# Performance work log

Hardware: AMD Instinct MI355X
Metric: run time of the kernel (lower is better)

The kernel has to match this reference:

```python
import jax, jax.numpy as jnp
import numpy as np

DIM = 256
HEADS = 8
HEAD_DIM = DIM // HEADS
B = 8
HH, WW = 32, 32
N = HH * WW
TABLE = (2 * HH - 1) * (2 * WW - 1)  # 3969
CPB_HID = 512


def _l2norm(t, eps=1e-12):
    # matches torch F.normalize(dim=-1): x / max(||x||, eps)
    n = jnp.sqrt(jnp.sum(t * t, axis=-1, keepdims=True))
    return t / jnp.maximum(n, eps)


def setup_inputs() -> dict:
    key = jax.random.key(0)
    ks = jax.random.split(key, 12)
    x = jax.random.normal(ks[0], (B, N, DIM), dtype=jnp.float32)
    relative_pos_index = jax.random.randint(ks[1], (N, N), 0, TABLE)
    relative_coords_table = jax.random.normal(ks[2], (TABLE, 2), dtype=jnp.float32)
    s = 0.02
    qkv_w = jax.random.normal(ks[3], (3 * DIM, DIM), dtype=jnp.float32) * s
    qkv_b = jnp.zeros((3 * DIM,), dtype=jnp.float32)
    query_embedding = jax.random.normal(ks[4], (HEADS, 1, HEAD_DIM), dtype=jnp.float32) * s
    # temperature init: log(exp(1/0.24) - 1) so softplus(temperature) = 1/0.24
    temperature = jnp.full((HEADS, 1, 1), float(np.log(np.expm1(1.0 / 0.24))), dtype=jnp.float32)
    proj_w = jax.random.normal(ks[5], (DIM, DIM), dtype=jnp.float32) * s
    proj_b = jnp.zeros((DIM,), dtype=jnp.float32)
    cpb_fc1_w = jax.random.normal(ks[6], (CPB_HID, 2), dtype=jnp.float32) * s
    cpb_fc1_b = jnp.zeros((CPB_HID,), dtype=jnp.float32)
    cpb_fc2_w = jax.random.normal(ks[7], (HEADS, CPB_HID), dtype=jnp.float32) * s
    cpb_fc2_b = jnp.zeros((HEADS,), dtype=jnp.float32)
    return dict(x=x, H=HH, W=WW, relative_pos_index=relative_pos_index,
                relative_coords_table=relative_coords_table,
                qkv_w=qkv_w, qkv_b=qkv_b, query_embedding=query_embedding,
                temperature=temperature, proj_w=proj_w, proj_b=proj_b,
                cpb_fc1_w=cpb_fc1_w, cpb_fc1_b=cpb_fc1_b,
                cpb_fc2_w=cpb_fc2_w, cpb_fc2_b=cpb_fc2_b)


def reference(x, H, W, relative_pos_index, relative_coords_table,
              qkv_w, qkv_b, query_embedding, temperature,
              proj_w, proj_b, cpb_fc1_w, cpb_fc1_b, cpb_fc2_w, cpb_fc2_b):
    Bc, Nc, C = x.shape
    seq_length_scale = jnp.asarray(np.log(HH * WW), dtype=x.dtype)  # from init input_resolution
    # qkv projection -> [B, heads, N, head_dim] each
    qkv = (x @ qkv_w.T + qkv_b).reshape(Bc, Nc, 3 * HEADS, HEAD_DIM).transpose(0, 2, 1, 3)
    q, k, v = qkv[:, :HEADS], qkv[:, HEADS:2 * HEADS], qkv[:, 2 * HEADS:]
    # CPB relative position bias: small MLP over coord table, then NxN gather
    h = jax.nn.relu(relative_coords_table @ cpb_fc1_w.T + cpb_fc1_b)  # [T, 512]
    table = (h @ cpb_fc2_w.T + cpb_fc2_b).T                           # [heads, T]
    rel_bias = table[:, relative_pos_index.reshape(-1)].reshape(HEADS, Nc, Nc)
    # cosine attention with learned temperature
    qn = _l2norm(q) + query_embedding[None]                           # [B, heads, N, hd]
    scale = jax.nn.softplus(temperature) * seq_length_scale           # [heads, 1, 1]
    attn = jnp.einsum('bhnd,bhmd->bhnm', qn * scale[None], _l2norm(k)) + rel_bias[None]
    attn = jax.nn.softmax(attn, axis=-1)
    out = jnp.einsum('bhnm,bhmd->bhnd', attn, v).transpose(0, 2, 1, 3).reshape(Bc, Nc, C)
    return out @ proj_w.T + proj_b
```

## Files before the change

kernel.cpp:

```cpp
#include <hip/hip_runtime.h>
#include <hip/hip_bf16.h>
#include <cstddef>
#include <cstdint>

typedef float v4f __attribute__((ext_vector_type(4)));
typedef short v8s __attribute__((ext_vector_type(8)));

__device__ __forceinline__ short f2bf(float x) {
    __hip_bfloat16 h = __float2bfloat16(x);
    short s; __builtin_memcpy(&s, &h, 2); return s;
}
__device__ __forceinline__ float bf2f(short s) {
    __hip_bfloat16 h; __builtin_memcpy(&h, &s, 2);
    return __bfloat162float(h);
}
__device__ __forceinline__ void gld16(const void* g, void* l) {
    __builtin_amdgcn_global_load_lds(
        (const __attribute__((address_space(1))) unsigned int*)g,
        (__attribute__((address_space(3))) unsigned int*)l, 16, 0, 0);
}
#define MFMA(a,b,c) __builtin_amdgcn_mfma_f32_16x16x32_bf16((a),(b),(c),0,0,0)

__global__ __launch_bounds__(256)
void cpb_kernel(const float* __restrict__ rct,
                const float* __restrict__ fc1w, const float* __restrict__ fc1b,
                const float* __restrict__ fc2w, const float* __restrict__ fc2b,
                float* __restrict__ table)
{
    __shared__ float s1[128];
    __shared__ float sb[64];
    __shared__ float s2[8][64];
    int tid = threadIdx.x;
    int jc  = blockIdx.y;
    int j0  = jc * 64;
    if (tid < 128) s1[tid] = fc1w[j0*2 + tid];
    else if (tid < 192) sb[tid-128] = fc1b[j0 + tid - 128];
    for (int i = tid; i < 512; i += 256) s2[i >> 6][i & 63] = fc2w[(i>>6)*512 + j0 + (i & 63)];
    __syncthreads();
    int r = blockIdx.x * 256 + tid;
    bool ok = r < 3969;
    float c0 = ok ? rct[2*r]   : 0.f;
    float c1 = ok ? rct[2*r+1] : 0.f;
    float a[8] = {0,0,0,0,0,0,0,0};
    #pragma unroll 4
    for (int j = 0; j < 64; ++j) {
        float hv = fmaxf(c0*s1[2*j] + c1*s1[2*j+1] + sb[j], 0.0f);
        #pragma unroll
        for (int hh = 0; hh < 8; ++hh) a[hh] += hv * s2[hh][j];
    }
    if (ok) {
        #pragma unroll
        for (int hh = 0; hh < 8; ++hh)
            atomicAdd(&table[hh*3969 + r], a[hh] + (jc == 0 ? fc2b[hh] : 0.f));
    }
}

__global__ __launch_bounds__(256)
void bias_mat(const float* __restrict__ tblf, const int* __restrict__ rpi,
              float* __restrict__ biasM)
{
    __shared__ float tb[3969];
    int h   = blockIdx.x >> 6;
    int q16 = blockIdx.x & 63;
    int tid = threadIdx.x;
    int w = tid >> 6, lane = tid & 63, t = lane & 15, quad = lane >> 4;
    for (int i = tid; i < 3969; i += 256) tb[i] = tblf[h*3969 + i];
    __syncthreads();
    int row0 = q16*16 + quad*4;
    #pragma unroll 1
    for (int kk = 0; kk < 4; ++kk) {
        int kt = w*4 + kk;
        #pragma unroll
        for (int g = 0; g < 4; ++g) {
            v4f o;
            #pragma unroll
            for (int r = 0; r < 4; ++r) {
                int idx = rpi[(size_t)(row0 + r)*1024 + kt*64 + 4*t + g];
                o[r] = tb[idx] - 40.0f;
            }
            size_t base = ((((size_t)(h*64 + q16)*16 + kt)*4 + g)*64 + lane)*4;
            *(v4f*)(biasM + base) = o;
        }
    }
}

__global__ __launch_bounds__(256)
void split_kernel(const float* __restrict__ x,  short* __restrict__ xh,  short* __restrict__ xl,
                  const float* __restrict__ wq, short* __restrict__ wqh, short* __restrict__ wql,
                  const float* __restrict__ wp, short* __restrict__ wph, short* __restrict__ wpl)
{
    int bid = blockIdx.x;
    const float* src; short* dh; short* dl; int base8;
    if (bid < 1024)      { src = x;  dh = xh;  dl = xl;  base8 = bid * 256; }
    else if (bid < 1120) { src = wq; dh = wqh; dl = wql; base8 = (bid-1024) * 256; }
    else                 { src = wp; dh = wph; dl = wpl; base8 = (bid-1120) * 256; }
    int e0 = (base8 + (int)threadIdx.x) * 8;
    int m  = e0 >> 8;
    int k  = e0 & 255;
    int kt = k >> 6, c = (k >> 3) & 7;
    float4 f0 = *(const float4*)(src + e0);
    float4 f1 = *(const float4*)(src + e0 + 4);
    float v[8] = {f0.x,f0.y,f0.z,f0.w,f1.x,f1.y,f1.z,f1.w};
    v8s hi, lo;
    #pragma unroll
    for (int j = 0; j < 8; ++j) {
        short h = f2bf(v[j]);
        hi[j] = h;
        lo[j] = f2bf(v[j] - bf2f(h));
    }
    int dst = m*256 + kt*64 + ((c ^ (m & 7)) << 3);
    *(v8s*)&dh[dst] = hi;
    *(v8s*)&dl[dst] = lo;
}

template<int MODE, int PASSES>
__global__ __launch_bounds__(256)
void gemm_mfma(const short* __restrict__ Ahi, const short* __restrict__ Alo,
               const short* __restrict__ Whi, const short* __restrict__ Wlo,
               const float* __restrict__ bias, float* __restrict__ C,
               short* __restrict__ qhi, short* __restrict__ qlo,
               short* __restrict__ khi, short* __restrict__ klo,
               short* __restrict__ vt,
               const float* __restrict__ qe, const float* __restrict__ temp,
               int N)
{
    __shared__ __align__(16) char smem[49152];
    short* Ah = (short*)smem;
    short* Al = Ah + 128*64;
    short* Wh = Al + 128*64;
    short* Wl = Wh + 64*64;

    int tid  = threadIdx.x;
    int w    = tid >> 6;
    int lane = tid & 63;
    int t    = lane & 15;
    int quad = lane >> 4;
    int m0 = blockIdx.y * 128, n0 = blockIdx.x * 64;
    int Mw = (w >> 1) * 64, Nw = (w & 1) * 32;
    const bool onep = (PASSES == 1) || (MODE == 1 && n0 >= 512);

    v4f acc[4][2];
    #pragma unroll
    for (int mt = 0; mt < 4; ++mt)
        #pragma unroll
        for (int nt = 0; nt < 2; ++nt) acc[mt][nt] = (v4f){0,0,0,0};

    int lr8 = lane >> 3, lc8 = lane & 7;
    #pragma unroll 1
    for (int kt = 0; kt < 4; ++kt) {
        __syncthreads();
        #pragma unroll
        for (int i = 0; i < 4; ++i) {
            size_t grow = (size_t)(m0 + w*32 + i*8 + lr8) * 256 + kt*64 + lc8*8;
            int ls = (w*32 + i*8) * 64;
            gld16(Ahi + grow, Ah + ls);
            if (!onep) gld16(Alo + grow, Al + ls);
        }
        #pragma unroll
        for (int i = 0; i < 2; ++i) {
            size_t grow = (size_t)(n0 + w*16 + i*8 + lr8) * 256 + kt*64 + lc8*8;
            int ls = (w*16 + i*8) * 64;
            gld16(Whi + grow, Wh + ls);
            if (!onep) gld16(Wlo + grow, Wl + ls);
        }
        __syncthreads();
        #pragma unroll
        for (int kk = 0; kk < 2; ++kk) {
            int cp = ((kk*4 + quad) ^ (t & 7)) << 3;
            v8s bh8[2], bl8[2];
            #pragma unroll
            for (int nt = 0; nt < 2; ++nt) {
                int rowi = Nw + nt*16 + t;
                bh8[nt] = *(const v8s*)&Wh[rowi*64 + cp];
                if (!onep) bl8[nt] = *(const v8s*)&Wl[rowi*64 + cp];
            }
            #pragma unroll
            for (int mt = 0; mt < 4; ++mt) {
                int rowi = Mw + mt*16 + t;
                v8s ah = *(const v8s*)&Ah[rowi*64 + cp];
                v8s al;
                if (!onep) al = *(const v8s*)&Al[rowi*64 + cp];
                #pragma unroll
                for (int nt = 0; nt < 2; ++nt) {
                    acc[mt][nt] = MFMA(ah, bh8[nt], acc[mt][nt]);
                    if (!onep) {
                        acc[mt][nt] = MFMA(al, bh8[nt], acc[mt][nt]);
                        acc[mt][nt] = MFMA(ah, bl8[nt], acc[mt][nt]);
                    }
                }
            }
        }
    }

    #pragma unroll
    for (int nt = 0; nt < 2; ++nt) {
        float bv = bias[n0 + Nw + nt*16 + t];
        #pragma unroll
        for (int mt = 0; mt < 4; ++mt)
            #pragma unroll
            for (int r = 0; r < 4; ++r) acc[mt][nt][r] += bv;
    }

    if (MODE == 0) {
        #pragma unroll
        for (int mt = 0; mt < 4; ++mt)
            #pragma unroll
            for (int r = 0; r < 4; ++r) {
                int m = m0 + Mw + mt*16 + quad*4 + r;
                #pragma unroll
                for (int nt = 0; nt < 2; ++nt) {
                    int n = n0 + Nw + nt*16 + t;
                    C[(size_t)m * N + n] = acc[mt][nt][r];
                }
            }
    } else {
        int which = n0 >> 8;
        if (which < 2) {
            int head = ((n0 + Nw) >> 5) & 7;
            float scale = 0.f;
            if (which == 0)
                scale = log1pf(__expf(temp[head])) * 6.9314718055994531f;
            #pragma unroll
            for (int mt = 0; mt < 4; ++mt)
                #pragma unroll
                for (int r = 0; r < 4; ++r) {
                    float a0 = acc[mt][0][r], a1 = acc[mt][1][r];
                    float s = a0*a0 + a1*a1;
                    s += __shfl_xor(s, 1); s += __shfl_xor(s, 2);
                    s += __shfl_xor(s, 4); s += __shfl_xor(s, 8);
                    float inv = 1.0f / fmaxf(sqrtf(s), 1e-12f);
                    int m = m0 + Mw + mt*16 + quad*4 + r;
                    int b = m >> 10, nrow = m & 1023;
                    if (which == 0) {
                        size_t rowoff = (((size_t)b*8 + head)*1024 + nrow) * 32;
                        #pragma unroll
                        for (int nt = 0; nt < 2; ++nt) {
                            int d = nt*16 + t;
                            float val = (acc[mt][nt][r] * inv + qe[head*32 + d]) * scale;
                            short hb = f2bf(val);
                            qhi[rowoff + d] = hb;
                            qlo[rowoff + d] = f2bf(val - bf2f(hb));
                        }
                    } else {
                        int kk = nrow & 63;
                        int p  = (kk & 3)*16 + (kk >> 2);
                        int prow = (nrow & ~63) | p;
                        int swk = (kk >> 3) & 3;
                        size_t rowoff = (((size_t)b*8 + head)*1024 + prow) * 32;
                        #pragma unroll
                        for (int nt = 0; nt < 2; ++nt) {
                            int d = nt*16 + t;
                            int c = d >> 3;
                            int dpos = ((c ^ swk) << 3) | (d & 7);
                            float val = acc[mt][nt][r] * inv;
                            short hb = f2bf(val);
                            khi[rowoff + dpos] = hb;
                            klo[rowoff + dpos] = f2bf(val - bf2f(hb));
                        }
                    }
                }
        } else {
            __syncthreads();
            short* VT = (short*)smem;
            #pragma unroll
            for (int mt = 0; mt < 4; ++mt)
                #pragma unroll
                for (int nt = 0; nt < 2; ++nt) {
                    int cl = Nw + nt*16 + t;
                    #pragma unroll
                    for (int r = 0; r < 4; ++r) {
                        int rl = Mw + mt*16 + quad*4 + r;
                        VT[cl*136 + rl] = f2bf(acc[mt][nt][r]);
                    }
                }
            __syncthreads();
            int b = m0 >> 10;
            int keybase = m0 & 1023;
            int headbase = ((n0 - 512) >> 5) & 7;
            int cl = tid >> 2;
            int dim = cl & 31;
            int hd  = headbase + (cl >> 5);
            size_t obase = (((size_t)b*8 + hd)*32 + dim) * 1024 + keybase;
            #pragma unroll
            for (int p = 0; p < 4; ++p) {
                int ci  = (tid & 3) * 4 + p;
                int ktl = ci >> 3, c = ci & 7;
                v8s val = *(const v8s*)&VT[cl*136 + ktl*64 + c*8];
                *(v8s*)&vt[obase + ktl*64 + ((c ^ (dim & 7)) << 3)] = val;
            }
        }
    }
}

__global__ __launch_bounds__(256)
void attn_mfma(const short* __restrict__ qhi, const short* __restrict__ qlo,
               const short* __restrict__ khi, const short* __restrict__ klo,
               const short* __restrict__ vt,  const float* __restrict__ biasM,
               short* __restrict__ yhi)
{
    __shared__ __align__(16) short Khi_s[2][2048];
    __shared__ __align__(16) short Klo_s[2][2048];
    __shared__ __align__(16) short Vt_s[2][2048];
    __shared__ __align__(16) short Ps[4][16][68];

    int bh  = blockIdx.x >> 4;
    int qt  = blockIdx.x & 15;
    int h   = bh & 7;
    int b   = bh >> 3;
    int tid = threadIdx.x;
    int w    = tid >> 6;
    int lane = tid & 63;
    int t    = lane & 15;
    int quad = lane >> 4;

    size_t qoff = ((size_t)bh*1024 + qt*64 + w*16 + t) * 32 + quad*8;
    v8s qfh = *(const v8s*)(qhi + qoff);
    v8s qfl = *(const v8s*)(qlo + qoff);

    v4f Oacc[2] = {{0,0,0,0},{0,0,0,0}};
    float lsum[4] = {0,0,0,0};

    size_t kgbase = (size_t)bh * 32768;
    const float* bmb = biasM + ((size_t)(h*64 + qt*4 + w) * 16) * 1024 + lane*4;
    int qrow0 = qt*64 + w*16 + quad*4;
    int swzS = (quad ^ ((t >> 1) & 3)) << 3;
    int lr8 = lane >> 3, lc8 = lane & 7;

    gld16(khi + kgbase + w*512 + lane*8, &Khi_s[0][w*512]);
    gld16(klo + kgbase + w*512 + lane*8, &Klo_s[0][w*512]);
    gld16(vt + kgbase + (size_t)(w*8 + lr8)*1024 + lc8*8, &Vt_s[0][w*512]);
    v4f curb[4];
    #pragma unroll
    for (int g = 0; g < 4; ++g) curb[g] = *(const v4f*)(bmb + g*256);

    #pragma unroll 1
    for (int kt = 0; kt < 16; ++kt) {
        int cur = kt & 1;
        __syncthreads();
        v4f nxtb[4];
        if (kt < 15) {
            int nkt = kt + 1, nb = cur ^ 1;
            gld16(khi + kgbase + (size_t)nkt*2048 + w*512 + lane*8, &Khi_s[nb][w*512]);
            gld16(klo + kgbase + (size_t)nkt*2048 + w*512 + lane*8, &Klo_s[nb][w*512]);
            gld16(vt + kgbase + (size_t)(w*8 + lr8)*1024 + nkt*64 + lc8*8, &Vt_s[nb][w*512]);
            const float* bp = bmb + (size_t)nkt*1024;
            #pragma unroll
            for (int g = 0; g < 4; ++g) nxtb[g] = *(const v4f*)(bp + g*256);
        }

        v4f S[4];
        #pragma unroll
        for (int g = 0; g < 4; ++g) {
            v8s bh8 = *(const v8s*)&Khi_s[cur][(g*16 + t)*32 + swzS];
            v8s bl8 = *(const v8s*)&Klo_s[cur][(g*16 + t)*32 + swzS];
            v4f c = curb[g];
            c = MFMA(qfh, bh8, c);
            c = MFMA(qfl, bh8, c);
            c = MFMA(qfh, bl8, c);
            S[g] = c;
        }

        #pragma unroll
        for (int r = 0; r < 4; ++r) {
            float p0 = __expf(S[0][r]);
            float p1 = __expf(S[1][r]);
            float p2 = __expf(S[2][r]);
            float p3 = __expf(S[3][r]);
            lsum[r] += (p0 + p1) + (p2 + p3);
            uint2 pk;
            pk.x = (uint32_t)(uint16_t)f2bf(p0) | ((uint32_t)(uint16_t)f2bf(p1) << 16);
            pk.y = (uint32_t)(uint16_t)f2bf(p2) | ((uint32_t)(uint16_t)f2bf(p3) << 16);
            *(uint2*)&Ps[w][quad*4 + r][t*4] = pk;
        }

        #pragma unroll
        for (int ks = 0; ks < 2; ++ks) {
            v8s pf = *(const v8s*)&Ps[w][t][ks*32 + quad*8];
            int vsw = ((ks*4 + quad) ^ (t & 7)) << 3;
            #pragma unroll
            for (int g = 0; g < 2; ++g) {
                v8s vf = *(const v8s*)&Vt_s[cur][(g*16 + t)*64 + vsw];
                Oacc[g] = MFMA(pf, vf, Oacc[g]);
            }
        }
        #pragma unroll
        for (int g = 0; g < 4; ++g) curb[g] = nxtb[g];
    }

    #pragma unroll
    for (int r = 0; r < 4; ++r) {
        float l = lsum[r];
        l += __shfl_xor(l, 1); l += __shfl_xor(l, 2);
        l += __shfl_xor(l, 4); l += __shfl_xor(l, 8);
        float inv = 1.0f / l;
        int qrow = qrow0 + r;
        int m = b*1024 + qrow;
        size_t mbase = (size_t)m * 256;
        int mk = m & 7;
        #pragma unroll
        for (int g = 0; g < 2; ++g) {
            float o = Oacc[g][r] * inv;
            int c = h*4 + g*2 + (t >> 3);
            int chp = ((c ^ mk) << 3) | (t & 7);
            yhi[mbase + chp] = f2bf(o);
        }
    }
}

extern "C" void kernel_launch(void* const* d_in, const int* in_sizes, int n_in,
                              void* d_out, int out_size, void* d_ws, size_t ws_size,
                              hipStream_t stream)
{
    const float* x     = (const float*)d_in[0];
    const int*   rpi   = (const int*)d_in[3];
    const float* rct   = (const float*)d_in[4];
    const float* qkvw  = (const float*)d_in[5];
    const float* qkvb  = (const float*)d_in[6];
    const float* qe    = (const float*)d_in[7];
    const float* temp  = (const float*)d_in[8];
    const float* projw = (const float*)d_in[9];
    const float* projb = (const float*)d_in[10];
    const float* fc1w  = (const float*)d_in[11];
    const float* fc1b  = (const float*)d_in[12];
    const float* fc2w  = (const float*)d_in[13];
    const float* fc2b  = (const float*)d_in[14];

    char* p = (char*)d_ws;
    float* tblf  = (float*)p;  p += 131072;
    short* xh    = (short*)p;  p += 4194304;
    short* xl    = (short*)p;  p += 4194304;
    short* wqh   = (short*)p;  p += 393216;
    short* wql   = (short*)p;  p += 393216;
    short* wph   = (short*)p;  p += 131072;
    short* wpl   = (short*)p;  p += 131072;
    short* qh    = (short*)p;  p += 4194304;
    short* ql    = (short*)p;  p += 4194304;
    short* kh    = (short*)p;  p += 4194304;
    short* kl    = (short*)p;  p += 4194304;
    short* vt    = (short*)p;  p += 4194304;
    float* biasM = (float*)p;  p += 33554432;
    float* out   = (float*)d_out;

    hipMemsetAsync(tblf, 0, 8*3969*sizeof(float), stream);
    cpb_kernel<<<dim3(16,8), 256, 0, stream>>>(rct, fc1w, fc1b, fc2w, fc2b, tblf);

    bias_mat<<<512, 256, 0, stream>>>(tblf, rpi, biasM);

    split_kernel<<<1152, 256, 0, stream>>>(x, xh, xl, qkvw, wqh, wql, projw, wph, wpl);

    dim3 g1(768/64, 8192/128);
    gemm_mfma<1,3><<<g1, 256, 0, stream>>>(xh, xl, wqh, wql, qkvb, nullptr,
                                           qh, ql, kh, kl, vt, qe, temp, 768);

    attn_mfma<<<1024, 256, 0, stream>>>(qh, ql, kh, kl, vt, biasM, xh);

    dim3 g2(256/64, 8192/128);
    gemm_mfma<0,1><<<g2, 256, 0, stream>>>(xh, nullptr, wph, nullptr, projb, out,
                                           nullptr, nullptr, nullptr, nullptr,
                                           nullptr, nullptr, nullptr, 256);
}
```

Baseline: 170.3 us.

## Store relative-position bias as bf16 and fold log2e into exp2 softmax

The precomputed per-head NxN bias matrix is now written and read as bf16 instead of fp32, with the constant -40 offset dropped. This halves its write and read traffic in the bias and attention kernels. Log2(e) is folded into the bias table and the query scale (6.93 becomes 10), so the attention kernel can use the native exp2 instruction in place of exp. Float-to-bf16 conversions use a cheaper add-and-shift rounding (round-half-up) with perm packing. The risks are lost bias precision, slightly different rounding, and larger exponent values now that the offset is gone.

```diff
diff --git a/kernel.cpp b/kernel.cpp
--- a/kernel.cpp
+++ b/kernel.cpp
@@ -6,20 +6,31 @@
 typedef float v4f __attribute__((ext_vector_type(4)));
 typedef short v8s __attribute__((ext_vector_type(8)));
 
-__device__ __forceinline__ short f2bf(float x) {
-    __hip_bfloat16 h = __float2bfloat16(x);
-    short s; __builtin_memcpy(&s, &h, 2); return s;
-}
-__device__ __forceinline__ float bf2f(short s) {
-    __hip_bfloat16 h; __builtin_memcpy(&h, &s, 2);
-    return __bfloat162float(h);
-}
+__device__ __forceinline__ uint32_t fbits(float x){ uint32_t u; __builtin_memcpy(&u,&x,4); return u; }
+__device__ __forceinline__ float ffrom(uint32_t u){ float f; __builtin_memcpy(&f,&u,4); return f; }
+__device__ __forceinline__ short bf_rh(float x){ return (short)((fbits(x)+0x8000u)>>16); }
+__device__ __forceinline__ uint32_t pack_bf_rh(float a, float b){
+    uint32_t ua = fbits(a)+0x8000u, ub = fbits(b)+0x8000u;
+#if __has_builtin(__builtin_amdgcn_perm)
+    return __builtin_amdgcn_perm(ub, ua, 0x07060302u);
+#else
+    return (ua>>16) | (ub & 0xFFFF0000u);
+#endif
+}
+#if __has_builtin(__builtin_amdgcn_exp2f)
+#define EXP2(x) __builtin_amdgcn_exp2f(x)
+#else
+#define EXP2(x) exp2f(x)
+#endif
+
 __device__ __forceinline__ void gld16(const void* g, void* l) {
     __builtin_amdgcn_global_load_lds(
         (const __attribute__((address_space(1))) unsigned int*)g,
         (__attribute__((address_space(3))) unsigned int*)l, 16, 0, 0);
 }
 #define MFMA(a,b,c) __builtin_amdgcn_mfma_f32_16x16x32_bf16((a),(b),(c),0,0,0)
+
+#define LOG2E 1.4426950408889634f
 
 __global__ __launch_bounds__(256)
 void cpb_kernel(const float* __restrict__ rct,
@@ -57,14 +68,14 @@
 
 __global__ __launch_bounds__(256)
 void bias_mat(const float* __restrict__ tblf, const int* __restrict__ rpi,
-              float* __restrict__ biasM)
+              short* __restrict__ biasM)
 {
     __shared__ float tb[3969];
     int h   = blockIdx.x >> 6;
     int q16 = blockIdx.x & 63;
     int tid = threadIdx.x;
     int w = tid >> 6, lane = tid & 63, t = lane & 15, quad = lane >> 4;
-    for (int i = tid; i < 3969; i += 256) tb[i] = tblf[h*3969 + i];
+    for (int i = tid; i < 3969; i += 256) tb[i] = tblf[h*3969 + i] * LOG2E;
     __syncthreads();
     int row0 = q16*16 + quad*4;
     #pragma unroll 1
@@ -72,14 +83,15 @@
         int kt = w*4 + kk;
         #pragma unroll
         for (int g = 0; g < 4; ++g) {
-            v4f o;
-            #pragma unroll
-            for (int r = 0; r < 4; ++r) {
-                int idx = rpi[(size_t)(row0 + r)*1024 + kt*64 + 4*t + g];
-                o[r] = tb[idx] - 40.0f;
-            }
+            float o[4];
+            #pragma unroll
+            for (int r = 0; r < 4; ++r)
+                o[r] = tb[rpi[(size_t)(row0 + r)*1024 + kt*64 + 4*t + g]];
+            uint2 pk;
+            pk.x = pack_bf_rh(o[0], o[1]);
+            pk.y = pack_bf_rh(o[2], o[3]);
             size_t base = ((((size_t)(h*64 + q16)*16 + kt)*4 + g)*64 + lane)*4;
-            *(v4f*)(biasM + base) = o;
+            *(uint2*)(biasM + base) = pk;
         }
     }
 }
@@ -104,9 +116,9 @@
     v8s hi, lo;
     #pragma unroll
     for (int j = 0; j < 8; ++j) {
-        short h = f2bf(v[j]);
-        hi[j] = h;
-        lo[j] = f2bf(v[j] - bf2f(h));
+        uint32_t u1 = fbits(v[j]) + 0x8000u;
+        hi[j] = (short)(u1 >> 16);
+        lo[j] = bf_rh(v[j] - ffrom(u1 & 0xFFFF0000u));
     }
     int dst = m*256 + kt*64 + ((c ^ (m & 7)) << 3);
     *(v8s*)&dh[dst] = hi;
@@ -219,7 +231,7 @@
             int head = ((n0 + Nw) >> 5) & 7;
             float scale = 0.f;
             if (which == 0)
-                scale = log1pf(__expf(temp[head])) * 6.9314718055994531f;
+                scale = log1pf(__expf(temp[head])) * 10.0f;
             #pragma unroll
             for (int mt = 0; mt < 4; ++mt)
                 #pragma unroll
@@ -237,9 +249,9 @@
                         for (int nt = 0; nt < 2; ++nt) {
                             int d = nt*16 + t;
                             float val = (acc[mt][nt][r] * inv + qe[head*32 + d]) * scale;
-                            short hb = f2bf(val);
-                            qhi[rowoff + d] = hb;
-                            qlo[rowoff + d] = f2bf(val - bf2f(hb));
+                            uint32_t u1 = fbits(val) + 0x8000u;
+                            qhi[rowoff + d] = (short)(u1 >> 16);
+                            qlo[rowoff + d] = bf_rh(val - ffrom(u1 & 0xFFFF0000u));
                         }
                     } else {
                         int kk = nrow & 63;
@@ -253,9 +265,9 @@
                             int c = d >> 3;
                             int dpos = ((c ^ swk) << 3) | (d & 7);
                             float val = acc[mt][nt][r] * inv;
-                            short hb = f2bf(val);
-                            khi[rowoff + dpos] = hb;
-                            klo[rowoff + dpos] = f2bf(val - bf2f(hb));
+                            uint32_t u1 = fbits(val) + 0x8000u;
+                            khi[rowoff + dpos] = (short)(u1 >> 16);
+                            klo[rowoff + dpos] = bf_rh(val - ffrom(u1 & 0xFFFF0000u));
                         }
                     }
                 }
@@ -270,7 +282,7 @@
                     #pragma unroll
                     for (int r = 0; r < 4; ++r) {
                         int rl = Mw + mt*16 + quad*4 + r;
-                        VT[cl*136 + rl] = f2bf(acc[mt][nt][r]);
+                        VT[cl*136 + rl] = bf_rh(acc[mt][nt][r]);
                     }
                 }
             __syncthreads();
@@ -295,7 +307,7 @@
 __global__ __launch_bounds__(256)
 void attn_mfma(const short* __restrict__ qhi, const short* __restrict__ qlo,
                const short* __restrict__ khi, const short* __restrict__ klo,
-               const short* __restrict__ vt,  const float* __restrict__ biasM,
+               const short* __restrict__ vt,  const short* __restrict__ biasM,
                short* __restrict__ yhi)
 {
     __shared__ __align__(16) short Khi_s[2][2048];
@@ -321,7 +333,7 @@
     float lsum[4] = {0,0,0,0};
 
     size_t kgbase = (size_t)bh * 32768;
-    const float* bmb = biasM + ((size_t)(h*64 + qt*4 + w) * 16) * 1024 + lane*4;
+    const short* bmb = biasM + ((size_t)(h*64 + qt*4 + w) * 16) * 1024 + lane*4;
     int qrow0 = qt*64 + w*16 + quad*4;
     int swzS = (quad ^ ((t >> 1) & 3)) << 3;
     int lr8 = lane >> 3, lc8 = lane & 7;
@@ -329,23 +341,23 @@
     gld16(khi + kgbase + w*512 + lane*8, &Khi_s[0][w*512]);
     gld16(klo + kgbase + w*512 + lane*8, &Klo_s[0][w*512]);
     gld16(vt + kgbase + (size_t)(w*8 + lr8)*1024 + lc8*8, &Vt_s[0][w*512]);
-    v4f curb[4];
+    uint2 curb[4];
     #pragma unroll
-    for (int g = 0; g < 4; ++g) curb[g] = *(const v4f*)(bmb + g*256);
+    for (int g = 0; g < 4; ++g) curb[g] = *(const uint2*)(bmb + g*256);
 
     #pragma unroll 1
     for (int kt = 0; kt < 16; ++kt) {
         int cur = kt & 1;
         __syncthreads();
-        v4f nxtb[4];
+        uint2 nxtb[4];
         if (kt < 15) {
             int nkt = kt + 1, nb = cur ^ 1;
             gld16(khi + kgbase + (size_t)nkt*2048 + w*512 + lane*8, &Khi_s[nb][w*512]);
             gld16(klo + kgbase + (size_t)nkt*2048 + w*512 + lane*8, &Klo_s[nb][w*512]);
             gld16(vt + kgbase + (size_t)(w*8 + lr8)*1024 + nkt*64 + lc8*8, &Vt_s[nb][w*512]);
-            const float* bp = bmb + (size_t)nkt*1024;
-            #pragma unroll
-            for (int g = 0; g < 4; ++g) nxtb[g] = *(const v4f*)(bp + g*256);
+            const short* bp = bmb + (size_t)nkt*1024;
+            #pragma unroll
+            for (int g = 0; g < 4; ++g) nxtb[g] = *(const uint2*)(bp + g*256);
         }
 
         v4f S[4];
@@ -353,7 +365,11 @@
         for (int g = 0; g < 4; ++g) {
             v8s bh8 = *(const v8s*)&Khi_s[cur][(g*16 + t)*32 + swzS];
             v8s bl8 = *(const v8s*)&Klo_s[cur][(g*16 + t)*32 + swzS];
-            v4f c = curb[g];
+            v4f c;
+            c[0] = ffrom(curb[g].x << 16);
+            c[1] = ffrom(curb[g].x & 0xFFFF0000u);
+            c[2] = ffrom(curb[g].y << 16);
+            c[3] = ffrom(curb[g].y & 0xFFFF0000u);
             c = MFMA(qfh, bh8, c);
             c = MFMA(qfl, bh8, c);
             c = MFMA(qfh, bl8, c);
@@ -362,14 +378,14 @@
 
         #pragma unroll
         for (int r = 0; r < 4; ++r) {
-            float p0 = __expf(S[0][r]);
-            float p1 = __expf(S[1][r]);
-            float p2 = __expf(S[2][r]);
-            float p3 = __expf(S[3][r]);
+            float p0 = EXP2(S[0][r]);
+            float p1 = EXP2(S[1][r]);
+            float p2 = EXP2(S[2][r]);
+            float p3 = EXP2(S[3][r]);
             lsum[r] += (p0 + p1) + (p2 + p3);
             uint2 pk;
-            pk.x = (uint32_t)(uint16_t)f2bf(p0) | ((uint32_t)(uint16_t)f2bf(p1) << 16);
-            pk.y = (uint32_t)(uint16_t)f2bf(p2) | ((uint32_t)(uint16_t)f2bf(p3) << 16);
+            pk.x = pack_bf_rh(p0, p1);
+            pk.y = pack_bf_rh(p2, p3);
             *(uint2*)&Ps[w][quad*4 + r][t*4] = pk;
         }
 
@@ -402,7 +418,7 @@
             float o = Oacc[g][r] * inv;
             int c = h*4 + g*2 + (t >> 3);
             int chp = ((c ^ mk) << 3) | (t & 7);
-            yhi[mbase + chp] = f2bf(o);
+            yhi[mbase + chp] = bf_rh(o);
         }
     }
 }
@@ -438,7 +454,7 @@
     short* kh    = (short*)p;  p += 4194304;
     short* kl    = (short*)p;  p += 4194304;
     short* vt    = (short*)p;  p += 4194304;
-    float* biasM = (float*)p;  p += 33554432;
+    short* biasM = (short*)p;  p += 16777216;
     float* out   = (float*)d_out;
 
     hipMemsetAsync(tblf, 0, 8*3969*sizeof(float), stream);
```

Result: no change. 169.2 us (-0.6%).
